# Optimization experiments

Measured on AMD Instinct MI355X. Metric: run time of the kernel, lower is better.

Reference implementation:

```python
import jax, jax.numpy as jnp
import numpy as np

N = 131072          # collocation points per dataset
C_WAVE = 1.0        # wave speed c
DIMS = [2, 256, 256, 256, 256, 1]


def _glorot(k, shape):
    fan_in, fan_out = shape
    std = jnp.sqrt(2.0 / (fan_in + fan_out)).astype(jnp.float32)
    return std * jax.random.normal(k, shape, dtype=jnp.float32)


def setup_inputs() -> dict:
    key = jax.random.key(0)
    ks = jax.random.split(key, 16)
    inp = {}
    for i in range(5):
        inp[f"W{i}"] = _glorot(ks[i], (DIMS[i], DIMS[i + 1]))
        inp[f"b{i}"] = jnp.zeros((DIMS[i + 1],), jnp.float32)
    inp["tx_equation"] = jax.random.uniform(ks[10], (N, 2), dtype=jnp.float32)
    inp["tx_init"] = jax.random.uniform(ks[11], (N, 2), dtype=jnp.float32)
    # initial condition points have t=0 in practice; values don't affect the math pattern
    inp["tx_init"] = inp["tx_init"].at[:, 0].set(0.0)
    inp["tx_bound"] = jax.random.uniform(ks[12], (N, 2), dtype=jnp.float32)
    return inp


def _mlp(params, tx):
    # tanh MLP: (..., 2) -> (..., 1)
    h = tx
    for W, b in params[:-1]:
        h = jnp.tanh(h @ W + b)
    W, b = params[-1]
    return h @ W + b


def reference(W0, b0, W1, b1, W2, b2, W3, b3, W4, b4,
              tx_equation, tx_init, tx_bound):
    params = [(W0, b0), (W1, b1), (W2, b2), (W3, b3), (W4, b4)]

    def u_scalar(tx):  # tx: (2,) -> scalar u(t, x)
        return _mlp(params, tx[None, :])[0, 0]

    # PDE residual: u_tt - c^2 * u_xx via per-point Hessian diagonal (input_diagonal_hessian)
    hess = jax.vmap(jax.hessian(u_scalar))(tx_equation)      # (N, 2, 2)
    u_tt = hess[:, 0, 0]
    u_xx = hess[:, 1, 1]
    pde_residual = (u_tt - (C_WAVE ** 2) * u_xx)[:, None]     # (N, 1)

    # Initial conditions: u and du/dt (input_gradient)
    u_init, g = jax.vmap(jax.value_and_grad(u_scalar))(tx_init)  # (N,), (N, 2)
    u_phi = u_init[:, None]                                   # (N, 1)
    du_dt_psi = g[:, 0][:, None]                              # (N, 1)

    # Boundary: plain forward
    u_bound = _mlp(params, tx_bound)                          # (N, 1)

    return jnp.stack([pde_residual, u_phi, du_dt_psi, u_bound], axis=0)  # (4, N, 1)
```

## Files before the change

kernel.cpp:

```cpp
#include <hip/hip_runtime.h>
#include <math.h>

#define N_PTS 131072
#define HID   256

typedef __attribute__((ext_vector_type(8)))  _Float16 f16x8;
typedef __attribute__((ext_vector_type(4)))  float    f32x4;
typedef __attribute__((ext_vector_type(16))) float    f32x16;
typedef unsigned int u32;
typedef __attribute__((address_space(1))) const u32 gu32;
typedef __attribute__((address_space(3))) u32       lu32;

#define LDS_HI  0
#define LDS_W   65536
#define LDS_SZ  81920

__device__ __forceinline__ int act_off(int row, int kbyte) {
    return row * 512 + (kbyte ^ ((row & 7) << 4));
}
__device__ __forceinline__ void tanh_f1(float z, float& h, float& f1) {
    float s = __expf(2.0f * z);
    float r = __builtin_amdgcn_rcpf(s + 1.0f);
    h  = fmaf(-2.0f, r, 1.0f);
    f1 = (1.0f - h) * (1.0f + h);
}

__global__ void prep_w(const float* __restrict__ W1, const float* __restrict__ W2,
                       const float* __restrict__ W3, char* __restrict__ ws)
{
    int idx = blockIdx.x * 256 + threadIdx.x;
    int l = idx >> 16;
    int e = idx & 65535;
    int k = e >> 8, n = e & 255;
    const float* W = (l == 0) ? W1 : (l == 1) ? W2 : W3;
    float w = W[e];
    int slab = l * 16 + (k >> 4);
    int byte_in = ((k >> 3) & 1) * 4096 + n * 16 + (k & 7) * 2;
    *(_Float16*)(ws + (size_t)slab * 8192 + byte_in) = (_Float16)w;
}

template<int S, int PTS>
__global__ void __launch_bounds__(512, 4)
pinn_mfma(const float* __restrict__ W0, const float* __restrict__ b0,
          const float* __restrict__ b1, const float* __restrict__ b2,
          const float* __restrict__ b3,
          const float* __restrict__ W4, const float* __restrict__ b4,
          const char* __restrict__ wpre,
          const float* __restrict__ tx, float* __restrict__ out)
{
    extern __shared__ char lds[];
    const int tid  = threadIdx.x;
    const int lane = tid & 63;
    const int wid  = tid >> 6;
    const int wr   = wid & 1;
    const int wc   = wid >> 1;
    const int pbase = blockIdx.x * PTS;
    constexpr int CG = 512 / PTS;
    constexpr int NC = 256 / CG;
    const int ep  = tid / CG;
    const int ec0 = (tid % CG) * NC;

    __builtin_amdgcn_global_load_lds((gu32*)(wpre + tid * 16),
                                     (lu32*)(lds + LDS_W + tid * 16), 16, 0, 0);

    {
        const float tt = tx[2 * (pbase + ep) + 0];
        const float xx = tx[2 * (pbase + ep) + 1];
        for (int cb = ec0; cb < ec0 + NC; cb += 8) {
            alignas(16) float w0r[8], w1r[8], bb[8];
            *(f32x4*)&w0r[0] = *(const f32x4*)(W0 + cb);
            *(f32x4*)&w0r[4] = *(const f32x4*)(W0 + cb + 4);
            *(f32x4*)&w1r[0] = *(const f32x4*)(W0 + HID + cb);
            *(f32x4*)&w1r[4] = *(const f32x4*)(W0 + HID + cb + 4);
            *(f32x4*)&bb[0]  = *(const f32x4*)(b0 + cb);
            *(f32x4*)&bb[4]  = *(const f32x4*)(b0 + cb + 4);
            f16x8 vhi[S];
            #pragma unroll
            for (int j = 0; j < 8; ++j) {
                float z = fmaf(tt, w0r[j], fmaf(xx, w1r[j], bb[j]));
                float h, f1;
                tanh_f1(z, h, f1);
                vhi[0][j] = (_Float16)h;
                if (S == 2) {
                    vhi[1][j] = (_Float16)(f1 * w0r[j]);
                } else if (S == 4) {
                    float d1 = w0r[j] + w1r[j];
                    float d2 = w0r[j] - w1r[j];
                    float f2 = -2.0f * h * f1;
                    vhi[1][j] = (_Float16)(f1 * d1);
                    vhi[2][j] = (_Float16)(f1 * d2);
                    vhi[3][j] = (_Float16)(f2 * d1 * d2);
                }
            }
            #pragma unroll
            for (int s2 = 0; s2 < S; ++s2) {
                int row = ep * S + s2;
                *(f16x8*)(lds + LDS_HI + act_off(row, cb * 2)) = vhi[s2];
            }
        }
    }

    const int c0 = (wc * 2) * 32 + (lane & 31);
    float bcv[3][2];
    bcv[0][0] = b1[c0]; bcv[0][1] = b1[c0 + 32];
    bcv[1][0] = b2[c0]; bcv[1][1] = b2[c0 + 32];
    bcv[2][0] = b3[c0]; bcv[2][1] = b3[c0 + 32];

    asm volatile("s_waitcnt vmcnt(0) lgkmcnt(0)" ::: "memory");
    __builtin_amdgcn_sched_barrier(0);
    __builtin_amdgcn_s_barrier();
    __builtin_amdgcn_sched_barrier(0);

    #pragma unroll
    for (int l = 0; l < 3; ++l) {
        f32x16 acc[2][2];
        #pragma unroll
        for (int i = 0; i < 2; ++i)
            #pragma unroll
            for (int j = 0; j < 2; ++j)
                acc[i][j] = (f32x16){0.f,0.f,0.f,0.f,0.f,0.f,0.f,0.f,
                                     0.f,0.f,0.f,0.f,0.f,0.f,0.f,0.f};

        #pragma unroll
        for (int ph = 0; ph < 16; ++ph) {
            const int g = l * 16 + ph;
            if (ph > 0) {
                asm volatile("s_waitcnt vmcnt(0)" ::: "memory");
                __builtin_amdgcn_s_barrier();
                __builtin_amdgcn_sched_barrier(0);
            }
            if (g < 47) {
                __builtin_amdgcn_global_load_lds(
                    (gu32*)(wpre + (size_t)(g + 1) * 8192 + tid * 16),
                    (lu32*)(lds + LDS_W + ((g + 1) & 1) * 8192 + tid * 16), 16, 0, 0);
            }
            const int kbyte = ph * 32 + ((lane >> 5) << 4);
            f16x8 av[2], bv[2];
            #pragma unroll
            for (int i = 0; i < 2; ++i) {
                const int row = (wr * 2 + i) * 32 + (lane & 31);
                av[i] = *(const f16x8*)(lds + LDS_HI + act_off(row, kbyte));
            }
            const char* wb = lds + LDS_W + (g & 1) * 8192 + ((lane >> 5) << 12);
            #pragma unroll
            for (int j = 0; j < 2; ++j) {
                const int n = (wc * 2 + j) * 32 + (lane & 31);
                bv[j] = *(const f16x8*)(wb + n * 16);
            }
            __builtin_amdgcn_s_setprio(1);
            acc[0][0] = __builtin_amdgcn_mfma_f32_32x32x16_f16(av[0], bv[0], acc[0][0], 0, 0, 0);
            acc[0][1] = __builtin_amdgcn_mfma_f32_32x32x16_f16(av[0], bv[1], acc[0][1], 0, 0, 0);
            acc[1][0] = __builtin_amdgcn_mfma_f32_32x32x16_f16(av[1], bv[0], acc[1][0], 0, 0, 0);
            acc[1][1] = __builtin_amdgcn_mfma_f32_32x32x16_f16(av[1], bv[1], acc[1][1], 0, 0, 0);
            __builtin_amdgcn_s_setprio(0);
        }
        __builtin_amdgcn_s_barrier();

        #pragma unroll
        for (int i = 0; i < 2; ++i) {
            #pragma unroll
            for (int j = 0; j < 2; ++j) {
                const int colj = (wc * 2 + j) * 32 + (lane & 31);
                const float bias = bcv[l][j];
                const int rtb = (wr * 2 + i) * 32 + 4 * (lane >> 5);
                #pragma unroll
                for (int q = 0; q < 4; ++q) {
                    const int rb = rtb + 8 * q;
                    if (S == 4) {
                        float z0 = acc[i][j][4*q+0] + bias;
                        float z1 = acc[i][j][4*q+1];
                        float z2 = acc[i][j][4*q+2];
                        float zm = acc[i][j][4*q+3];
                        float h, f1;
                        tanh_f1(z0, h, f1);
                        float f2 = -2.0f * h * f1;
                        *(_Float16*)(lds + LDS_HI + act_off(rb+0, colj*2)) = (_Float16)h;
                        *(_Float16*)(lds + LDS_HI + act_off(rb+1, colj*2)) = (_Float16)(f1 * z1);
                        *(_Float16*)(lds + LDS_HI + act_off(rb+2, colj*2)) = (_Float16)(f1 * z2);
                        *(_Float16*)(lds + LDS_HI + act_off(rb+3, colj*2)) =
                            (_Float16)(fmaf(f1, zm, f2 * z1 * z2));
                    } else if (S == 2) {
                        #pragma unroll
                        for (int pp = 0; pp < 2; ++pp) {
                            float z0 = acc[i][j][4*q+2*pp+0] + bias;
                            float zd = acc[i][j][4*q+2*pp+1];
                            float h, f1;
                            tanh_f1(z0, h, f1);
                            *(_Float16*)(lds + LDS_HI + act_off(rb+2*pp+0, colj*2)) = (_Float16)h;
                            *(_Float16*)(lds + LDS_HI + act_off(rb+2*pp+1, colj*2)) = (_Float16)(f1 * zd);
                        }
                    } else {
                        #pragma unroll
                        for (int m = 0; m < 4; ++m) {
                            float z0 = acc[i][j][4*q+m] + bias;
                            float h, f1;
                            tanh_f1(z0, h, f1);
                            *(_Float16*)(lds + LDS_HI + act_off(rb+m, colj*2)) = (_Float16)h;
                        }
                    }
                }
            }
        }
        asm volatile("s_waitcnt vmcnt(0) lgkmcnt(0)" ::: "memory");
        __builtin_amdgcn_sched_barrier(0);
        __builtin_amdgcn_s_barrier();
        __builtin_amdgcn_sched_barrier(0);
    }

    if (S == 4) {
        const int p   = tid >> 4;
        const int seg = tid & 15;
        const int k0  = seg * 16;
        const int row = 4 * p + 3;
        float d = 0.0f;
        #pragma unroll
        for (int kb = 0; kb < 16; kb += 8) {
            f16x8 h8 = *(const f16x8*)(lds + LDS_HI + act_off(row, (k0 + kb) * 2));
            alignas(16) float wv[8];
            *(f32x4*)&wv[0] = *(const f32x4*)(W4 + k0 + kb);
            *(f32x4*)&wv[4] = *(const f32x4*)(W4 + k0 + kb + 4);
            #pragma unroll
            for (int j = 0; j < 8; ++j) d = fmaf((float)h8[j], wv[j], d);
        }
        #pragma unroll
        for (int off = 8; off > 0; off >>= 1) d += __shfl_down(d, off, 16);
        if (seg == 0) out[0 * N_PTS + pbase + p] = d;
    } else {
        const int row = tid >> 2;
        const int seg = tid & 3;
        const int k0  = seg * 64;
        float d = 0.0f;
        #pragma unroll
        for (int kb = 0; kb < 64; kb += 8) {
            f16x8 h8 = *(const f16x8*)(lds + LDS_HI + act_off(row, (k0 + kb) * 2));
            alignas(16) float wv[8];
            *(f32x4*)&wv[0] = *(const f32x4*)(W4 + k0 + kb);
            *(f32x4*)&wv[4] = *(const f32x4*)(W4 + k0 + kb + 4);
            #pragma unroll
            for (int j = 0; j < 8; ++j) d = fmaf((float)h8[j], wv[j], d);
        }
        d += __shfl_down(d, 2, 4);
        d += __shfl_down(d, 1, 4);
        if (seg == 0) {
            if (S == 2) {
                const int p = row >> 1;
                if ((row & 1) == 0) out[1 * N_PTS + pbase + p] = d + b4[0];
                else                out[2 * N_PTS + pbase + p] = d;
            } else {
                out[3 * N_PTS + pbase + row] = d + b4[0];
            }
        }
    }
}

extern "C" void kernel_launch(void* const* d_in, const int* in_sizes, int n_in,
                              void* d_out, int out_size, void* d_ws, size_t ws_size,
                              hipStream_t stream) {
    const float* W0 = (const float*)d_in[0];
    const float* b0 = (const float*)d_in[1];
    const float* W1 = (const float*)d_in[2];
    const float* b1 = (const float*)d_in[3];
    const float* W2 = (const float*)d_in[4];
    const float* b2 = (const float*)d_in[5];
    const float* W3 = (const float*)d_in[6];
    const float* b3 = (const float*)d_in[7];
    const float* W4 = (const float*)d_in[8];
    const float* b4 = (const float*)d_in[9];
    const float* tx_eq    = (const float*)d_in[10];
    const float* tx_init  = (const float*)d_in[11];
    const float* tx_bound = (const float*)d_in[12];
    float* out = (float*)d_out;
    char* wpre = (char*)d_ws;

    hipFuncSetAttribute((const void*)pinn_mfma<4,32>,  hipFuncAttributeMaxDynamicSharedMemorySize, LDS_SZ);
    hipFuncSetAttribute((const void*)pinn_mfma<2,64>,  hipFuncAttributeMaxDynamicSharedMemorySize, LDS_SZ);
    hipFuncSetAttribute((const void*)pinn_mfma<1,128>, hipFuncAttributeMaxDynamicSharedMemorySize, LDS_SZ);

    prep_w<<<768, 256, 0, stream>>>(W1, W2, W3, wpre);
    pinn_mfma<4,32> <<<N_PTS/32,  512, LDS_SZ, stream>>>(W0,b0,b1,b2,b3,W4,b4,wpre,tx_eq,   out);
    pinn_mfma<2,64> <<<N_PTS/64,  512, LDS_SZ, stream>>>(W0,b0,b1,b2,b3,W4,b4,wpre,tx_init, out);
    pinn_mfma<1,128><<<N_PTS/128, 512, LDS_SZ, stream>>>(W0,b0,b1,b2,b3,W4,b4,wpre,tx_bound,out);
}
```

Before: 685.0 us.

## Halve block size to 256 threads and 64 rows to raise occupancy

Shrinks each block from 8 waves over 128 activation rows to 4 waves over 64 rows, with each wave now covering all rows for a 64-column slice. LDS per block drops from 80KB to 48KB so several blocks fit per CU, and each thread stages two 16-byte weight chunks per slab. This should let more waves overlap the barrier-synchronised weight streaming. In exchange, each weight slab is reused by half as many points, which doubles global weight traffic and the number of block-wide barriers per point.

```diff
diff --git a/kernel.cpp b/kernel.cpp
--- a/kernel.cpp
+++ b/kernel.cpp
@@ -12,8 +12,8 @@
 typedef __attribute__((address_space(3))) u32       lu32;
 
 #define LDS_HI  0
-#define LDS_W   65536
-#define LDS_SZ  81920
+#define LDS_W   32768
+#define LDS_SZ  49152
 
 __device__ __forceinline__ int act_off(int row, int kbyte) {
     return row * 512 + (kbyte ^ ((row & 7) << 4));
@@ -39,8 +39,17 @@
     *(_Float16*)(ws + (size_t)slab * 8192 + byte_in) = (_Float16)w;
 }
 
+__device__ __forceinline__ void stage_slab(const char* __restrict__ src,
+                                           char* dst, int tid) {
+    #pragma unroll
+    for (int q = 0; q < 2; ++q) {
+        __builtin_amdgcn_global_load_lds((gu32*)(src + q * 4096 + tid * 16),
+                                         (lu32*)(dst + q * 4096 + tid * 16), 16, 0, 0);
+    }
+}
+
 template<int S, int PTS>
-__global__ void __launch_bounds__(512, 4)
+__global__ void __launch_bounds__(256, 3)
 pinn_mfma(const float* __restrict__ W0, const float* __restrict__ b0,
           const float* __restrict__ b1, const float* __restrict__ b2,
           const float* __restrict__ b3,
@@ -52,16 +61,13 @@
     const int tid  = threadIdx.x;
     const int lane = tid & 63;
     const int wid  = tid >> 6;
-    const int wr   = wid & 1;
-    const int wc   = wid >> 1;
     const int pbase = blockIdx.x * PTS;
-    constexpr int CG = 512 / PTS;
+    constexpr int CG = 256 / PTS;
     constexpr int NC = 256 / CG;
     const int ep  = tid / CG;
     const int ec0 = (tid % CG) * NC;
 
-    __builtin_amdgcn_global_load_lds((gu32*)(wpre + tid * 16),
-                                     (lu32*)(lds + LDS_W + tid * 16), 16, 0, 0);
+    stage_slab(wpre, lds + LDS_W, tid);
 
     {
         const float tt = tx[2 * (pbase + ep) + 0];
@@ -100,7 +106,7 @@
         }
     }
 
-    const int c0 = (wc * 2) * 32 + (lane & 31);
+    const int c0 = wid * 64 + (lane & 31);
     float bcv[3][2];
     bcv[0][0] = b1[c0]; bcv[0][1] = b1[c0 + 32];
     bcv[1][0] = b2[c0]; bcv[1][1] = b2[c0 + 32];
@@ -130,21 +136,20 @@
                 __builtin_amdgcn_sched_barrier(0);
             }
             if (g < 47) {
-                __builtin_amdgcn_global_load_lds(
-                    (gu32*)(wpre + (size_t)(g + 1) * 8192 + tid * 16),
-                    (lu32*)(lds + LDS_W + ((g + 1) & 1) * 8192 + tid * 16), 16, 0, 0);
+                stage_slab(wpre + (size_t)(g + 1) * 8192,
+                           lds + LDS_W + ((g + 1) & 1) * 8192, tid);
             }
             const int kbyte = ph * 32 + ((lane >> 5) << 4);
             f16x8 av[2], bv[2];
             #pragma unroll
             for (int i = 0; i < 2; ++i) {
-                const int row = (wr * 2 + i) * 32 + (lane & 31);
+                const int row = i * 32 + (lane & 31);
                 av[i] = *(const f16x8*)(lds + LDS_HI + act_off(row, kbyte));
             }
             const char* wb = lds + LDS_W + (g & 1) * 8192 + ((lane >> 5) << 12);
             #pragma unroll
             for (int j = 0; j < 2; ++j) {
-                const int n = (wc * 2 + j) * 32 + (lane & 31);
+                const int n = wid * 64 + j * 32 + (lane & 31);
                 bv[j] = *(const f16x8*)(wb + n * 16);
             }
             __builtin_amdgcn_s_setprio(1);
@@ -160,9 +165,9 @@
         for (int i = 0; i < 2; ++i) {
             #pragma unroll
             for (int j = 0; j < 2; ++j) {
-                const int colj = (wc * 2 + j) * 32 + (lane & 31);
+                const int colj = wid * 64 + j * 32 + (lane & 31);
                 const float bias = bcv[l][j];
-                const int rtb = (wr * 2 + i) * 32 + 4 * (lane >> 5);
+                const int rtb = i * 32 + 4 * (lane >> 5);
                 #pragma unroll
                 for (int q = 0; q < 4; ++q) {
                     const int rb = rtb + 8 * q;
@@ -272,12 +277,8 @@
     float* out = (float*)d_out;
     char* wpre = (char*)d_ws;
 
-    hipFuncSetAttribute((const void*)pinn_mfma<4,32>,  hipFuncAttributeMaxDynamicSharedMemorySize, LDS_SZ);
-    hipFuncSetAttribute((const void*)pinn_mfma<2,64>,  hipFuncAttributeMaxDynamicSharedMemorySize, LDS_SZ);
-    hipFuncSetAttribute((const void*)pinn_mfma<1,128>, hipFuncAttributeMaxDynamicSharedMemorySize, LDS_SZ);
-
     prep_w<<<768, 256, 0, stream>>>(W1, W2, W3, wpre);
-    pinn_mfma<4,32> <<<N_PTS/32,  512, LDS_SZ, stream>>>(W0,b0,b1,b2,b3,W4,b4,wpre,tx_eq,   out);
-    pinn_mfma<2,64> <<<N_PTS/64,  512, LDS_SZ, stream>>>(W0,b0,b1,b2,b3,W4,b4,wpre,tx_init, out);
-    pinn_mfma<1,128><<<N_PTS/128, 512, LDS_SZ, stream>>>(W0,b0,b1,b2,b3,W4,b4,wpre,tx_bound,out);
-}
+    pinn_mfma<4,16><<<N_PTS/16, 256, LDS_SZ, stream>>>(W0,b0,b1,b2,b3,W4,b4,wpre,tx_eq,   out);
+    pinn_mfma<2,32><<<N_PTS/32, 256, LDS_SZ, stream>>>(W0,b0,b1,b2,b3,W4,b4,wpre,tx_init, out);
+    pinn_mfma<1,64><<<N_PTS/64, 256, LDS_SZ, stream>>>(W0,b0,b1,b2,b3,W4,b4,wpre,tx_bound,out);
+}
```

Result: faster. 563.7 us (-17.7%).
